# Kernel tuning notes

Hardware: AMD Instinct MI355X
Metric: run time of the kernel (lower is better)

## Reference

```python
import jax, jax.numpy as jnp
import numpy as np

DIM = 1024
NUM_HEADS = 16
HEAD_DIM = DIM // NUM_HEADS


def setup_inputs() -> dict:
    key = jax.random.key(0)
    k_x, k_qkv, k_proj, k_b = jax.random.split(key, 4)
    B, N, P, C = 4, 96, 64, DIM
    x = jax.random.normal(k_x, (B, N, P, C), dtype=jnp.float32)
    # nn.Linear(dim, 3*dim, bias=False): store as (in, out) for x @ W
    s = 1.0 / np.sqrt(C)
    W_qkv = jax.random.uniform(k_qkv, (C, 3 * C), minval=-s, maxval=s, dtype=jnp.float32)
    W_proj = jax.random.uniform(k_proj, (C, C), minval=-s, maxval=s, dtype=jnp.float32)
    b_proj = jax.random.uniform(k_b, (C,), minval=-s, maxval=s, dtype=jnp.float32)
    return {"x": x, "W_qkv": W_qkv, "W_proj": W_proj, "b_proj": b_proj}


def reference(x, W_qkv, W_proj, b_proj):
    B, N, P, C = x.shape
    H, hd = NUM_HEADS, C // NUM_HEADS
    # qkv projection: (B,N,P,3C) -> (B,N,P,3,H,hd)
    qkv = (x @ W_qkv).reshape(B, N, P, 3, H, hd)
    # q,k: mean-pool over patches P -> (B,H,N,hd)
    q = qkv[..., 0, :, :].mean(axis=2).transpose(0, 2, 1, 3)
    k = qkv[..., 1, :, :].mean(axis=2).transpose(0, 2, 1, 3)
    # v keeps all patches: (B,N,P,H,hd) -> (B,H,N,hd,P) -> (B,H,N,hd*P)
    v = qkv[..., 2, :, :].transpose(0, 3, 1, 4, 2).reshape(B, H, N, hd * P)
    # SDPA with default scale 1/sqrt(q_last_dim) = 1/sqrt(hd)
    scores = jnp.einsum('bhnd,bhmd->bhnm', q, k) * (hd ** -0.5)
    attn = jax.nn.softmax(scores, axis=-1)
    out = jnp.einsum('bhnm,bhme->bhne', attn, v)  # e = hd*P
    # unflatten back to (B,N,P,C)
    out = out.reshape(B, H, N, hd, P).transpose(0, 2, 4, 1, 3).reshape(B, N, P, C)
    return out @ W_proj + b_proj
```

## Files before the change

kernel.cpp:

```cpp
#include <hip/hip_runtime.h>
#include <cstdint>
#include <cstddef>

#define PPP  64
#define CC   1024

typedef __attribute__((ext_vector_type(8))) short short8;
typedef __attribute__((ext_vector_type(4))) float floatx4;
typedef __attribute__((ext_vector_type(4))) unsigned short ushort4v;

__device__ inline float bf2f(unsigned short u) {
  union { unsigned int i; float f; } v; v.i = ((unsigned int)u) << 16; return v.f;
}
__device__ inline unsigned short f2bf(float f) {
  union { float f; unsigned int i; } v; v.f = f;
  unsigned int x = v.i;
  unsigned int r = (x + 0x7fffu + ((x >> 16) & 1u)) >> 16;
  return (unsigned short)r;
}

#define GLD16(gp, lp)                                                          \
  __builtin_amdgcn_global_load_lds(                                            \
      (const __attribute__((address_space(1))) void*)(gp),                     \
      (__attribute__((address_space(3))) void*)(lp), 16, 0, 0)

__global__ __launch_bounds__(256) void conv_mean(
    const float* __restrict__ x, unsigned short* __restrict__ xbf,
    unsigned short* __restrict__ xm) {
  int bn = blockIdx.x;
  int c4 = threadIdx.x * 4;
  const float* xp = x + (size_t)bn * (PPP * CC) + c4;
  unsigned short* xo = xbf + (size_t)bn * (PPP * CC) + c4;
  float4 s = {0.f, 0.f, 0.f, 0.f};
#pragma unroll 8
  for (int p = 0; p < PPP; ++p) {
    float4 v = *(const float4*)&xp[(size_t)p * CC];
    s.x += v.x; s.y += v.y; s.z += v.z; s.w += v.w;
    ushort4v pk;
    pk.x = f2bf(v.x); pk.y = f2bf(v.y); pk.z = f2bf(v.z); pk.w = f2bf(v.w);
    *(ushort4v*)&xo[(size_t)p * CC] = pk;
  }
  ushort4v pm;
  pm.x = f2bf(s.x * (1.0f / PPP)); pm.y = f2bf(s.y * (1.0f / PPP));
  pm.z = f2bf(s.z * (1.0f / PPP)); pm.w = f2bf(s.w * (1.0f / PPP));
  *(ushort4v*)&xm[(size_t)bn * CC + c4] = pm;
}

__global__ __launch_bounds__(256) void transpose_f32_bf16(
    const float* __restrict__ src, unsigned short* __restrict__ dst,
    int R, int Cc, int src_stride) {
  __shared__ unsigned short tile[32][33];
  int tc = blockIdx.x * 32, tr = blockIdx.y * 32;
  int tx = threadIdx.x & 31, ty = threadIdx.x >> 5;
  for (int yy = ty; yy < 32; yy += 8)
    tile[yy][tx] = f2bf(src[(size_t)(tr + yy) * src_stride + tc + tx]);
  __syncthreads();
  for (int yy = ty; yy < 32; yy += 8)
    dst[(size_t)(tc + yy) * R + tr + tx] = tile[tx][yy];
}

template <bool F32OUT, bool SWIZ>
__global__ __launch_bounds__(256) void gemm_bt(
    const unsigned short* __restrict__ A, const unsigned short* __restrict__ BT,
    void* __restrict__ Cout, const float* __restrict__ bias,
    int M, int N, int K, int nbx) {
  __shared__ unsigned short As[128 * 32];
  __shared__ unsigned short Bs[128 * 32];

  int bx, by;
  {
    int bid = blockIdx.x;
    if (SWIZ) {
      bx = (bid >> 3) & 7;
      by = (bid & 7) * (gridDim.x >> 6) + (bid >> 6);
    } else {
      bx = bid % nbx;
      by = bid / nbx;
    }
  }
  const int rowBase = by * 128;
  const int colBase = bx * 128;
  const int t = threadIdx.x;
  const int wave = t >> 6, lane = t & 63;
  const int qr = wave >> 1, qc = wave & 1;
  const int m16 = lane & 15, quad = lane >> 4;

  floatx4 acc[4][4];
#pragma unroll
  for (int i = 0; i < 4; ++i)
#pragma unroll
    for (int j = 0; j < 4; ++j) {
      acc[i][j][0] = 0.f; acc[i][j][1] = 0.f; acc[i][j][2] = 0.f; acc[i][j][3] = 0.f;
    }

  for (int k0 = 0; k0 < K; k0 += 32) {
    __syncthreads();
#pragma unroll
    for (int u = 0; u < 2; ++u) {
      int ch = (u * 4 + wave) * 64 + lane;
      int row = ch >> 2, c8 = (ch & 3) << 3;
      GLD16(&A [(size_t)(rowBase + row) * K + k0 + c8], &As[ch * 8]);
      GLD16(&BT[(size_t)(colBase + row) * K + k0 + c8], &Bs[ch * 8]);
    }
    __syncthreads();

    short8 af[4], bfr[4];
#pragma unroll
    for (int i = 0; i < 4; ++i)
      af[i] = *(const short8*)&As[(qr * 64 + i * 16 + m16) * 32 + quad * 8];
#pragma unroll
    for (int j = 0; j < 4; ++j)
      bfr[j] = *(const short8*)&Bs[(qc * 64 + j * 16 + m16) * 32 + quad * 8];
#pragma unroll
    for (int i = 0; i < 4; ++i)
#pragma unroll
      for (int j = 0; j < 4; ++j)
        acc[i][j] = __builtin_amdgcn_mfma_f32_16x16x32_bf16(af[i], bfr[j], acc[i][j], 0, 0, 0);
  }

  float bv[4];
#pragma unroll
  for (int j = 0; j < 4; ++j)
    bv[j] = bias ? bias[colBase + qc * 64 + j * 16 + m16] : 0.f;

#pragma unroll
  for (int i = 0; i < 4; ++i) {
    int row0 = rowBase + qr * 64 + i * 16 + quad * 4;
#pragma unroll
    for (int j = 0; j < 4; ++j) {
      int col = colBase + qc * 64 + j * 16 + m16;
#pragma unroll
      for (int r = 0; r < 4; ++r) {
        float f = acc[i][j][r] + bv[j];
        if (F32OUT)
          ((float*)Cout)[(size_t)(row0 + r) * N + col] = f;
        else
          ((unsigned short*)Cout)[(size_t)(row0 + r) * N + col] = f2bf(f);
      }
    }
  }
}

__global__ __launch_bounds__(128) void softmax_k(
    const float* __restrict__ qk, unsigned short* __restrict__ attn) {
  int bh = blockIdx.x;
  int b = bh >> 4, h = bh & 15;
  __shared__ float ks[96][64];
  __shared__ float sc[96][96];
  int t = threadIdx.x;
  for (int idx = t; idx < 96 * 64; idx += 128) {
    int n = idx >> 6, d = idx & 63;
    ks[n][d] = qk[(size_t)(b * 96 + n) * 2048 + 1024 + h * 64 + d];
  }
  __syncthreads();
  if (t < 96) {
    float qreg[64];
    const float* qrow = qk + (size_t)(b * 96 + t) * 2048 + h * 64;
#pragma unroll
    for (int d = 0; d < 64; ++d) qreg[d] = qrow[d];

    float mx = -1e30f;
    for (int m = 0; m < 96; ++m) {
      float s0 = 0.f, s1 = 0.f, s2 = 0.f, s3 = 0.f;
#pragma unroll
      for (int d = 0; d < 64; d += 4) {
        s0 += qreg[d + 0] * ks[m][d + 0];
        s1 += qreg[d + 1] * ks[m][d + 1];
        s2 += qreg[d + 2] * ks[m][d + 2];
        s3 += qreg[d + 3] * ks[m][d + 3];
      }
      float s = ((s0 + s1) + (s2 + s3)) * 0.125f;
      sc[m][t] = s;
      mx = fmaxf(mx, s);
    }
    float sum = 0.f;
    for (int m = 0; m < 96; ++m) {
      float e = __expf(sc[m][t] - mx);
      sc[m][t] = e;
      sum += e;
    }
    float inv = 1.0f / sum;
    size_t base = (size_t)(bh * 96 + t) * 96;
    for (int m = 0; m < 96; ++m) attn[base + m] = f2bf(sc[m][t] * inv);
  }
}

__global__ __launch_bounds__(256) void attn_apply_mfma(
    const unsigned short* __restrict__ attn, const unsigned short* __restrict__ V,
    unsigned short* __restrict__ out2) {
  const int bid = blockIdx.x;
  const int bh = bid >> 5, ct = bid & 31;
  const int b = bh >> 4;
  const int t = threadIdx.x;
  const int wave = t >> 6, lane = t & 63;
  const int m16 = lane & 15, quad = lane >> 4;

  const unsigned short* An = attn + (size_t)bh * 96 * 96;
  const int vb = b * 96 * 64 * CC;

  floatx4 acc[6][2];
#pragma unroll
  for (int i = 0; i < 6; ++i)
#pragma unroll
    for (int j = 0; j < 2; ++j) {
      acc[i][j][0] = 0.f; acc[i][j][1] = 0.f; acc[i][j][2] = 0.f; acc[i][j][3] = 0.f;
    }

  int p_[2], base_[2];
#pragma unroll
  for (int jj = 0; jj < 2; ++jj) {
    int colL = wave * 32 + jj * 16;
    int p = ct * 2 + (colL >> 6);
    int d = (colL & 63) + m16;
    p_[jj] = p;
    base_[jj] = vb + p * CC + ((bh & 15) * 64) + d;
  }

#pragma unroll
  for (int k0 = 0; k0 < 96; k0 += 32) {
    short8 af[6];
#pragma unroll
    for (int i = 0; i < 6; ++i)
      af[i] = *(const short8*)&An[(i * 16 + m16) * 96 + k0 + quad * 8];
#pragma unroll
    for (int jj = 0; jj < 2; ++jj) {
      short8 bfr;
#pragma unroll
      for (int j = 0; j < 8; ++j)
        bfr[j] = (short)V[(size_t)base_[jj] + (size_t)(k0 + quad * 8 + j) * (64 * CC)];
#pragma unroll
      for (int i = 0; i < 6; ++i)
        acc[i][jj] = __builtin_amdgcn_mfma_f32_16x16x32_bf16(af[i], bfr, acc[i][jj], 0, 0, 0);
    }
  }

#pragma unroll
  for (int jj = 0; jj < 2; ++jj) {
    int colL = wave * 32 + jj * 16;
    int d = (colL & 63) + m16;
    size_t obase = (size_t)(b * 96) * 64 * CC + (size_t)p_[jj] * CC + (bh & 15) * 64 + d;
#pragma unroll
    for (int i = 0; i < 6; ++i) {
#pragma unroll
      for (int r = 0; r < 4; ++r) {
        int n = i * 16 + quad * 4 + r;
        out2[obase + (size_t)n * (64 * CC)] = f2bf(acc[i][jj][r]);
      }
    }
  }
}

extern "C" void kernel_launch(void* const* d_in, const int* in_sizes, int n_in,
                              void* d_out, int out_size, void* d_ws, size_t ws_size,
                              hipStream_t stream) {
  const float* x      = (const float*)d_in[0];
  const float* W_qkv  = (const float*)d_in[1];
  const float* W_proj = (const float*)d_in[2];
  const float* b_proj = (const float*)d_in[3];
  float* out = (float*)d_out;

  char* w = (char*)d_ws;
  unsigned short* WqkvT = (unsigned short*)(w);
  unsigned short* WpT   = (unsigned short*)(w + 6291456);
  unsigned short* xm    = (unsigned short*)(w + 8388608);
  float*          qkbuf = (float*)(w + 9175040);
  unsigned short* attn  = (unsigned short*)(w + 12320768);
  unsigned short* out2w = (unsigned short*)(w + 13500416);
  unsigned short* xbf   = (unsigned short*)d_out;
  unsigned short* Vbuf  = (unsigned short*)((char*)d_out + 50331648);

  const bool fullws = ws_size >= (size_t)13500416 + 50331648;

  conv_mean<<<dim3(384), 256, 0, stream>>>(x, xbf, xm);

  transpose_f32_bf16<<<dim3(96, 32), 256, 0, stream>>>(W_qkv, WqkvT, 1024, 3072, 3072);
  transpose_f32_bf16<<<dim3(32, 32), 256, 0, stream>>>(W_proj, WpT, 1024, 1024, 1024);

  gemm_bt<true, false><<<dim3(48), 256, 0, stream>>>(
      xm, WqkvT, qkbuf, nullptr, 384, 2048, 1024, 16);

  softmax_k<<<dim3(64), 128, 0, stream>>>(qkbuf, attn);

  gemm_bt<false, true><<<dim3(1536), 256, 0, stream>>>(
      xbf, WqkvT + (size_t)2048 * 1024, Vbuf, nullptr, 24576, 1024, 1024, 8);

  if (fullws) {
    attn_apply_mfma<<<dim3(2048), 256, 0, stream>>>(attn, Vbuf, out2w);
    gemm_bt<true, true><<<dim3(1536), 256, 0, stream>>>(
        out2w, WpT, out, b_proj, 24576, 1024, 1024, 8);
  } else {
    for (int b = 0; b < 4; ++b) {
      attn_apply_mfma<<<dim3(512), 256, 0, stream>>>(
          attn + (size_t)b * 16 * 96 * 96,
          Vbuf + (size_t)b * 6144 * 1024,
          out2w);
      gemm_bt<true, true><<<dim3(384), 256, 0, stream>>>(
          out2w, WpT, out + (size_t)b * 6144 * 1024, b_proj, 6144, 1024, 1024, 8);
    }
  }
}
```

Baseline: 407.5 us.

## Add 256x128-tile triple-buffered MFMA GEMM for the large V and output projections

```diff
diff --git a/kernel.cpp b/kernel.cpp
--- a/kernel.cpp
+++ b/kernel.cpp
@@ -141,6 +141,149 @@
   }
 }
 
+template <bool F32OUT>
+__global__ __launch_bounds__(512, 2) void gemm_bt256(
+    const unsigned short* __restrict__ A, const unsigned short* __restrict__ BT,
+    void* __restrict__ Cout, const float* __restrict__ bias,
+    int M, int N, int K) {
+  __shared__ __attribute__((aligned(16))) unsigned short As[3][256 * 64];
+  __shared__ __attribute__((aligned(16))) unsigned short Bs[3][128 * 64];
+
+  const int nbx = N >> 7;
+  int tid = (blockIdx.x & 7) * (gridDim.x >> 3) + (blockIdx.x >> 3);
+  const int bx = tid % nbx, by = tid / nbx;
+  const int rowBase = by * 256;
+  const int colBase = bx * 128;
+
+  const int t = threadIdx.x;
+  const int wave = t >> 6, lane = t & 63;
+  const int wr = wave >> 1, wc = wave & 1;
+  const int m16 = lane & 15, quad = lane >> 4;
+  const int sw7 = lane & 7;
+
+  const unsigned short* srcA[4];
+  const unsigned short* srcB[2];
+  int offA[4], offB[2];
+#pragma unroll
+  for (int u = 0; u < 4; ++u) {
+    int c = (u * 8 + wave) * 64 + lane;
+    int row = c >> 3, pch = c & 7;
+    int l = pch ^ (row & 7);
+    srcA[u] = A + (size_t)(rowBase + row) * K + l * 8;
+    offA[u] = c * 8;
+  }
+#pragma unroll
+  for (int u = 0; u < 2; ++u) {
+    int c = (u * 8 + wave) * 64 + lane;
+    int row = c >> 3, pch = c & 7;
+    int l = pch ^ (row & 7);
+    srcB[u] = BT + (size_t)(colBase + row) * K + l * 8;
+    offB[u] = c * 8;
+  }
+
+  floatx4 acc[4][4];
+#pragma unroll
+  for (int i = 0; i < 4; ++i)
+#pragma unroll
+    for (int j = 0; j < 4; ++j) {
+      acc[i][j][0] = 0.f; acc[i][j][1] = 0.f; acc[i][j][2] = 0.f; acc[i][j][3] = 0.f;
+    }
+
+  const int NT = K >> 6;
+
+#pragma unroll
+  for (int u = 0; u < 4; ++u) GLD16(srcA[u], &As[0][offA[u]]);
+#pragma unroll
+  for (int u = 0; u < 2; ++u) GLD16(srcB[u], &Bs[0][offB[u]]);
+#pragma unroll
+  for (int u = 0; u < 4; ++u) GLD16(srcA[u] + 64, &As[1][offA[u]]);
+#pragma unroll
+  for (int u = 0; u < 2; ++u) GLD16(srcB[u] + 64, &Bs[1][offB[u]]);
+
+#define LDA_F(Ac, i, kh) \
+  (*(const short8*)&(Ac)[(wr * 64 + (i) * 16 + m16) * 64 + ((((kh) * 4 + quad) ^ sw7) * 8)])
+#define LDB_F(Bc, j, kh) \
+  (*(const short8*)&(Bc)[(wc * 64 + (j) * 16 + m16) * 64 + ((((kh) * 4 + quad) ^ sw7) * 8)])
+
+  int cur = 0, nb = 2;
+#pragma unroll 1
+  for (int kt = 0; kt < NT; ++kt) {
+    if (kt == NT - 1)
+      asm volatile("s_waitcnt vmcnt(0)" ::: "memory");
+    else
+      asm volatile("s_waitcnt vmcnt(6)" ::: "memory");
+    asm volatile("s_barrier" ::: "memory");
+
+    const unsigned short* Ac = &As[cur][0];
+    const unsigned short* Bc = &Bs[cur][0];
+    const bool st = (kt + 2) < NT;
+    const int koff = (kt + 2) << 6;
+
+#pragma unroll
+    for (int p = 0; p < 4; ++p) {
+      const int i0 = (p >> 1) * 2, i1 = i0 + 1;
+      const int j0 = (p & 1) * 2, j1 = j0 + 1;
+      short8 A00 = LDA_F(Ac, i0, 0), A01 = LDA_F(Ac, i0, 1);
+      short8 A10 = LDA_F(Ac, i1, 0), A11 = LDA_F(Ac, i1, 1);
+      short8 B00 = LDB_F(Bc, j0, 0), B01 = LDB_F(Bc, j0, 1);
+      short8 B10 = LDB_F(Bc, j1, 0), B11 = LDB_F(Bc, j1, 1);
+      if (st) {
+        if (p == 0) {
+          GLD16(srcA[0] + koff, &As[nb][offA[0]]);
+          GLD16(srcA[1] + koff, &As[nb][offA[1]]);
+        } else if (p == 1) {
+          GLD16(srcA[2] + koff, &As[nb][offA[2]]);
+          GLD16(srcA[3] + koff, &As[nb][offA[3]]);
+        } else if (p == 2) {
+          GLD16(srcB[0] + koff, &Bs[nb][offB[0]]);
+        } else {
+          GLD16(srcB[1] + koff, &Bs[nb][offB[1]]);
+        }
+      }
+      asm volatile("s_barrier" ::: "memory");
+      __builtin_amdgcn_sched_barrier(0);
+      __builtin_amdgcn_s_setprio(1);
+      acc[i0][j0] = __builtin_amdgcn_mfma_f32_16x16x32_bf16(A00, B00, acc[i0][j0], 0, 0, 0);
+      acc[i0][j0] = __builtin_amdgcn_mfma_f32_16x16x32_bf16(A01, B01, acc[i0][j0], 0, 0, 0);
+      acc[i0][j1] = __builtin_amdgcn_mfma_f32_16x16x32_bf16(A00, B10, acc[i0][j1], 0, 0, 0);
+      acc[i0][j1] = __builtin_amdgcn_mfma_f32_16x16x32_bf16(A01, B11, acc[i0][j1], 0, 0, 0);
+      acc[i1][j0] = __builtin_amdgcn_mfma_f32_16x16x32_bf16(A10, B00, acc[i1][j0], 0, 0, 0);
+      acc[i1][j0] = __builtin_amdgcn_mfma_f32_16x16x32_bf16(A11, B01, acc[i1][j0], 0, 0, 0);
+      acc[i1][j1] = __builtin_amdgcn_mfma_f32_16x16x32_bf16(A10, B10, acc[i1][j1], 0, 0, 0);
+      acc[i1][j1] = __builtin_amdgcn_mfma_f32_16x16x32_bf16(A11, B11, acc[i1][j1], 0, 0, 0);
+      __builtin_amdgcn_s_setprio(0);
+      __builtin_amdgcn_sched_barrier(0);
+      asm volatile("s_barrier" ::: "memory");
+    }
+    cur = (cur == 2) ? 0 : cur + 1;
+    nb = (nb == 2) ? 0 : nb + 1;
+  }
+#undef LDA_F
+#undef LDB_F
+
+  float bv[4];
+#pragma unroll
+  for (int j = 0; j < 4; ++j)
+    bv[j] = bias ? bias[colBase + wc * 64 + j * 16 + m16] : 0.f;
+
+#pragma unroll
+  for (int i = 0; i < 4; ++i) {
+    int row0 = rowBase + wr * 64 + i * 16 + quad * 4;
+#pragma unroll
+    for (int j = 0; j < 4; ++j) {
+      int col = colBase + wc * 64 + j * 16 + m16;
+#pragma unroll
+      for (int r = 0; r < 4; ++r) {
+        float f = acc[i][j][r] + bv[j];
+        if (F32OUT)
+          ((float*)Cout)[(size_t)(row0 + r) * N + col] = f;
+        else
+          ((unsigned short*)Cout)[(size_t)(row0 + r) * N + col] = f2bf(f);
+      }
+    }
+  }
+}
+
 __global__ __launch_bounds__(128) void softmax_k(
     const float* __restrict__ qk, unsigned short* __restrict__ attn) {
   int bh = blockIdx.x;
@@ -281,21 +424,21 @@
 
   softmax_k<<<dim3(64), 128, 0, stream>>>(qkbuf, attn);
 
-  gemm_bt<false, true><<<dim3(1536), 256, 0, stream>>>(
-      xbf, WqkvT + (size_t)2048 * 1024, Vbuf, nullptr, 24576, 1024, 1024, 8);
+  gemm_bt256<false><<<dim3(768), 512, 0, stream>>>(
+      xbf, WqkvT + (size_t)2048 * 1024, Vbuf, nullptr, 24576, 1024, 1024);
 
   if (fullws) {
     attn_apply_mfma<<<dim3(2048), 256, 0, stream>>>(attn, Vbuf, out2w);
-    gemm_bt<true, true><<<dim3(1536), 256, 0, stream>>>(
-        out2w, WpT, out, b_proj, 24576, 1024, 1024, 8);
+    gemm_bt256<true><<<dim3(768), 512, 0, stream>>>(
+        out2w, WpT, out, b_proj, 24576, 1024, 1024);
   } else {
     for (int b = 0; b < 4; ++b) {
       attn_apply_mfma<<<dim3(512), 256, 0, stream>>>(
           attn + (size_t)b * 16 * 96 * 96,
           Vbuf + (size_t)b * 6144 * 1024,
           out2w);
-      gemm_bt<true, true><<<dim3(384), 256, 0, stream>>>(
-          out2w, WpT, out + (size_t)b * 6144 * 1024, b_proj, 6144, 1024, 1024, 8);
-    }
-  }
-}
+      gemm_bt256<true><<<dim3(192), 512, 0, stream>>>(
+          out2w, WpT, out + (size_t)b * 6144 * 1024, b_proj, 6144, 1024, 1024);
+    }
+  }
+}
```

Result: slower. 434.5 us (+6.6%).

## Add 256x256-tile bf16 GEMM with phased double-buffered pipeline for V and proj

Applied to the files above, without the earlier changes.

```diff
diff --git a/kernel.cpp b/kernel.cpp
--- a/kernel.cpp
+++ b/kernel.cpp
@@ -141,6 +141,161 @@
   }
 }
 
+template <bool F32OUT>
+__global__ __launch_bounds__(512, 2) void gemm_bt256(
+    const unsigned short* __restrict__ A, const unsigned short* __restrict__ BT,
+    void* __restrict__ Cout, const float* __restrict__ bias,
+    int M, int N, int K) {
+  __shared__ __attribute__((aligned(16))) unsigned short As[2][256 * 64];
+  __shared__ __attribute__((aligned(16))) unsigned short Bs[2][256 * 64];
+
+  const int nbx = N >> 8;
+  int tid = (blockIdx.x & 7) * (gridDim.x >> 3) + (blockIdx.x >> 3);
+  const int bx = tid % nbx, by = tid / nbx;
+  const int rowBase = by * 256, colBase = bx * 256;
+
+  const int t = threadIdx.x;
+  const int wave = t >> 6, lane = t & 63;
+  const int wr = wave >> 2, wc = wave & 3;
+  const int m16 = lane & 15, quad = lane >> 4;
+  const int sw7 = m16 & 7;
+
+  const unsigned short* srcA[4];
+  int offA[4];
+#pragma unroll
+  for (int u = 0; u < 4; ++u) {
+    int c = u * 512 + t;
+    int row = c >> 3, pch = c & 7;
+    int l = pch ^ (row & 7);
+    srcA[u] = A + (size_t)(rowBase + row) * K + l * 8;
+    offA[u] = c * 8;
+  }
+  const unsigned short* srcB[2][2];
+  int offB[2][2];
+#pragma unroll
+  for (int g = 0; g < 2; ++g)
+#pragma unroll
+    for (int u = 0; u < 2; ++u) {
+      int i = u * 512 + t;
+      int col = g * 32 + ((i >> 8) << 6) + ((i >> 3) & 31);
+      int kcp = i & 7;
+      int l = kcp ^ (col & 7);
+      srcB[g][u] = BT + (size_t)(colBase + col) * K + l * 8;
+      offB[g][u] = col * 64 + kcp * 8;
+    }
+
+  floatx4 acc[8][4];
+#pragma unroll
+  for (int i = 0; i < 8; ++i)
+#pragma unroll
+    for (int j = 0; j < 4; ++j) {
+      acc[i][j][0] = 0.f; acc[i][j][1] = 0.f; acc[i][j][2] = 0.f; acc[i][j][3] = 0.f;
+    }
+
+  short8 ar[4][2];
+  short8 br[2][2][2];
+
+#define RD_A(buf, qa)                                                          \
+  _Pragma("unroll") for (int i_ = 0; i_ < 4; ++i_)                             \
+  _Pragma("unroll") for (int kh_ = 0; kh_ < 2; ++kh_)                          \
+    ar[i_][kh_] = *(const short8*)&As[buf][                                    \
+        (wr * 128 + (qa) * 64 + i_ * 16 + m16) * 64 +                          \
+        (((kh_ * 4 + quad) ^ sw7) * 8)];
+#define RD_B(buf, qb)                                                          \
+  _Pragma("unroll") for (int j_ = 0; j_ < 2; ++j_)                             \
+  _Pragma("unroll") for (int kh_ = 0; kh_ < 2; ++kh_)                          \
+    br[qb][j_][kh_] = *(const short8*)&Bs[buf][                                \
+        (wc * 64 + (qb) * 32 + j_ * 16 + m16) * 64 +                           \
+        (((kh_ * 4 + quad) ^ sw7) * 8)];
+#define MFMA_PH(qa, qb)                                                        \
+  __builtin_amdgcn_sched_barrier(0);                                           \
+  __builtin_amdgcn_s_setprio(1);                                               \
+  _Pragma("unroll") for (int kh_ = 0; kh_ < 2; ++kh_)                          \
+  _Pragma("unroll") for (int i_ = 0; i_ < 4; ++i_)                             \
+  _Pragma("unroll") for (int j_ = 0; j_ < 2; ++j_)                             \
+    acc[(qa) * 4 + i_][(qb) * 2 + j_] =                                        \
+        __builtin_amdgcn_mfma_f32_16x16x32_bf16(                               \
+            ar[i_][kh_], br[qb][j_][kh_], acc[(qa) * 4 + i_][(qb) * 2 + j_],   \
+            0, 0, 0);                                                          \
+  __builtin_amdgcn_s_setprio(0);                                               \
+  __builtin_amdgcn_sched_barrier(0);
+#define WAITV(n) asm volatile("s_waitcnt vmcnt(" #n ")" ::: "memory")
+#define BAR() asm volatile("s_barrier" ::: "memory")
+
+  GLD16(srcA[0], &As[0][offA[0]]);
+  GLD16(srcA[2], &As[0][offA[2]]);
+  GLD16(srcB[0][0], &Bs[0][offB[0][0]]);
+  GLD16(srcB[0][1], &Bs[0][offB[0][1]]);
+  GLD16(srcB[1][0], &Bs[0][offB[1][0]]);
+  GLD16(srcB[1][1], &Bs[0][offB[1][1]]);
+  GLD16(srcA[1], &As[0][offA[1]]);
+  GLD16(srcA[3], &As[0][offA[3]]);
+
+  const int NT = K >> 6;
+  int cur = 0;
+#pragma unroll 1
+  for (int kt = 0; kt < NT - 1; ++kt, cur ^= 1) {
+    const int nxt = cur ^ 1;
+    const int ko = (kt + 1) << 6;
+    WAITV(4); BAR();
+    RD_A(cur, 0); RD_B(cur, 0);
+    GLD16(srcA[0] + ko, &As[nxt][offA[0]]);
+    GLD16(srcA[2] + ko, &As[nxt][offA[2]]);
+    MFMA_PH(0, 0);
+    WAITV(4); BAR();
+    RD_B(cur, 1);
+    GLD16(srcB[0][0] + ko, &Bs[nxt][offB[0][0]]);
+    GLD16(srcB[0][1] + ko, &Bs[nxt][offB[0][1]]);
+    MFMA_PH(0, 1);
+    WAITV(4); BAR();
+    RD_A(cur, 1);
+    GLD16(srcB[1][0] + ko, &Bs[nxt][offB[1][0]]);
+    GLD16(srcB[1][1] + ko, &Bs[nxt][offB[1][1]]);
+    MFMA_PH(1, 0);
+    GLD16(srcA[1] + ko, &As[nxt][offA[1]]);
+    GLD16(srcA[3] + ko, &As[nxt][offA[3]]);
+    MFMA_PH(1, 1);
+  }
+  WAITV(4); BAR();
+  RD_A(cur, 0); RD_B(cur, 0);
+  MFMA_PH(0, 0);
+  WAITV(2); BAR();
+  RD_B(cur, 1);
+  MFMA_PH(0, 1);
+  WAITV(0); BAR();
+  RD_A(cur, 1);
+  MFMA_PH(1, 0);
+  MFMA_PH(1, 1);
+
+#undef RD_A
+#undef RD_B
+#undef MFMA_PH
+#undef WAITV
+#undef BAR
+
+  float bv[4];
+#pragma unroll
+  for (int jg = 0; jg < 4; ++jg)
+    bv[jg] = bias ? bias[colBase + wc * 64 + jg * 16 + m16] : 0.f;
+
+#pragma unroll
+  for (int ig = 0; ig < 8; ++ig) {
+    int row0 = rowBase + wr * 128 + ig * 16 + quad * 4;
+#pragma unroll
+    for (int jg = 0; jg < 4; ++jg) {
+      int col = colBase + wc * 64 + jg * 16 + m16;
+#pragma unroll
+      for (int r = 0; r < 4; ++r) {
+        float f = acc[ig][jg][r] + bv[jg];
+        if (F32OUT)
+          ((float*)Cout)[(size_t)(row0 + r) * N + col] = f;
+        else
+          ((unsigned short*)Cout)[(size_t)(row0 + r) * N + col] = f2bf(f);
+      }
+    }
+  }
+}
+
 __global__ __launch_bounds__(128) void softmax_k(
     const float* __restrict__ qk, unsigned short* __restrict__ attn) {
   int bh = blockIdx.x;
@@ -281,21 +436,21 @@
 
   softmax_k<<<dim3(64), 128, 0, stream>>>(qkbuf, attn);
 
-  gemm_bt<false, true><<<dim3(1536), 256, 0, stream>>>(
-      xbf, WqkvT + (size_t)2048 * 1024, Vbuf, nullptr, 24576, 1024, 1024, 8);
+  gemm_bt256<false><<<dim3(384), 512, 0, stream>>>(
+      xbf, WqkvT + (size_t)2048 * 1024, Vbuf, nullptr, 24576, 1024, 1024);
 
   if (fullws) {
     attn_apply_mfma<<<dim3(2048), 256, 0, stream>>>(attn, Vbuf, out2w);
-    gemm_bt<true, true><<<dim3(1536), 256, 0, stream>>>(
-        out2w, WpT, out, b_proj, 24576, 1024, 1024, 8);
+    gemm_bt256<true><<<dim3(384), 512, 0, stream>>>(
+        out2w, WpT, out, b_proj, 24576, 1024, 1024);
   } else {
     for (int b = 0; b < 4; ++b) {
       attn_apply_mfma<<<dim3(512), 256, 0, stream>>>(
           attn + (size_t)b * 16 * 96 * 96,
           Vbuf + (size_t)b * 6144 * 1024,
           out2w);
-      gemm_bt<true, true><<<dim3(384), 256, 0, stream>>>(
-          out2w, WpT, out + (size_t)b * 6144 * 1024, b_proj, 6144, 1024, 1024, 8);
-    }
-  }
-}
+      gemm_bt256<true><<<dim3(96), 512, 0, stream>>>(
+          out2w, WpT, out + (size_t)b * 6144 * 1024, b_proj, 6144, 1024, 1024);
+    }
+  }
+}
```

Result: faster. 386.5 us (-5.2%).

## Add 128x256-tile double-buffered bf16 GEMM for the two large projections

Applied to the files above, without the earlier changes.

```diff
diff --git a/kernel.cpp b/kernel.cpp
--- a/kernel.cpp
+++ b/kernel.cpp
@@ -141,6 +141,113 @@
   }
 }
 
+template <bool F32OUT>
+__global__ __launch_bounds__(256, 2) void gemm_bt128(
+    const unsigned short* __restrict__ A, const unsigned short* __restrict__ BT,
+    void* __restrict__ Cout, const float* __restrict__ bias,
+    int M, int N, int K) {
+  __shared__ __attribute__((aligned(16))) unsigned short As[2][128 * 32];
+  __shared__ __attribute__((aligned(16))) unsigned short Bs[2][256 * 32];
+
+  const int nbx = N >> 8;
+  int tid = (blockIdx.x & 7) * (gridDim.x >> 3) + (blockIdx.x >> 3);
+  const int bx = tid % nbx, by = tid / nbx;
+  const int rowBase = by * 128, colBase = bx * 256;
+
+  const int t = threadIdx.x;
+  const int wave = t >> 6, lane = t & 63;
+  const int m16 = lane & 15, quad = lane >> 4;
+  const int ck = quad ^ ((m16 >> 1) & 3);
+
+  const unsigned short* srcA[2]; int offA[2];
+#pragma unroll
+  for (int u = 0; u < 2; ++u) {
+    int c = u * 256 + t;
+    int row = c >> 2, pch = c & 3;
+    int l = pch ^ ((row >> 1) & 3);
+    srcA[u] = A + (size_t)(rowBase + row) * K + l * 8;
+    offA[u] = c * 8;
+  }
+  const unsigned short* srcB[4]; int offB[4];
+#pragma unroll
+  for (int u = 0; u < 4; ++u) {
+    int c = u * 256 + t;
+    int row = c >> 2, pch = c & 3;
+    int l = pch ^ ((row >> 1) & 3);
+    srcB[u] = BT + (size_t)(colBase + row) * K + l * 8;
+    offB[u] = c * 8;
+  }
+
+  floatx4 acc[8][4];
+#pragma unroll
+  for (int i = 0; i < 8; ++i)
+#pragma unroll
+    for (int j = 0; j < 4; ++j) {
+      acc[i][j][0] = 0.f; acc[i][j][1] = 0.f; acc[i][j][2] = 0.f; acc[i][j][3] = 0.f;
+    }
+
+#define WAITV0() asm volatile("s_waitcnt vmcnt(0)" ::: "memory")
+#define BARR()   asm volatile("s_barrier" ::: "memory")
+
+#pragma unroll
+  for (int u = 0; u < 2; ++u) GLD16(srcA[u], &As[0][offA[u]]);
+#pragma unroll
+  for (int u = 0; u < 4; ++u) GLD16(srcB[u], &Bs[0][offB[u]]);
+
+  const int NT = K >> 5;
+  int cur = 0;
+#pragma unroll 1
+  for (int kt = 0; kt < NT; ++kt, cur ^= 1) {
+    WAITV0(); BARR();
+    if (kt + 1 < NT) {
+      const int ko = (kt + 1) << 5;
+      const int nxt = cur ^ 1;
+#pragma unroll
+      for (int u = 0; u < 2; ++u) GLD16(srcA[u] + ko, &As[nxt][offA[u]]);
+#pragma unroll
+      for (int u = 0; u < 4; ++u) GLD16(srcB[u] + ko, &Bs[nxt][offB[u]]);
+    }
+    short8 af[8], bfr[4];
+#pragma unroll
+    for (int i = 0; i < 8; ++i)
+      af[i] = *(const short8*)&As[cur][(i * 16 + m16) * 32 + ck * 8];
+#pragma unroll
+    for (int j = 0; j < 4; ++j)
+      bfr[j] = *(const short8*)&Bs[cur][(wave * 64 + j * 16 + m16) * 32 + ck * 8];
+    __builtin_amdgcn_s_setprio(1);
+#pragma unroll
+    for (int i = 0; i < 8; ++i)
+#pragma unroll
+      for (int j = 0; j < 4; ++j)
+        acc[i][j] = __builtin_amdgcn_mfma_f32_16x16x32_bf16(af[i], bfr[j], acc[i][j], 0, 0, 0);
+    __builtin_amdgcn_s_setprio(0);
+  }
+#undef WAITV0
+#undef BARR
+
+  float bv[4];
+#pragma unroll
+  for (int jg = 0; jg < 4; ++jg)
+    bv[jg] = bias ? bias[colBase + wave * 64 + jg * 16 + m16] : 0.f;
+
+#pragma unroll
+  for (int ig = 0; ig < 8; ++ig) {
+    int row0 = rowBase + ig * 16 + quad * 4;
+#pragma unroll
+    for (int jg = 0; jg < 4; ++jg) {
+      int col = colBase + wave * 64 + jg * 16 + m16;
+#pragma unroll
+      for (int r = 0; r < 4; ++r) {
+        float f = acc[ig][jg][r] + bv[jg];
+        if (F32OUT)
+          ((float*)Cout)[(size_t)(row0 + r) * N + col] = f;
+        else
+          ((unsigned short*)Cout)[(size_t)(row0 + r) * N + col] = f2bf(f);
+      }
+    }
+  }
+}
+
 __global__ __launch_bounds__(128) void softmax_k(
     const float* __restrict__ qk, unsigned short* __restrict__ attn) {
   int bh = blockIdx.x;
@@ -281,21 +388,21 @@
 
   softmax_k<<<dim3(64), 128, 0, stream>>>(qkbuf, attn);
 
-  gemm_bt<false, true><<<dim3(1536), 256, 0, stream>>>(
-      xbf, WqkvT + (size_t)2048 * 1024, Vbuf, nullptr, 24576, 1024, 1024, 8);
+  gemm_bt128<false><<<dim3(768), 256, 0, stream>>>(
+      xbf, WqkvT + (size_t)2048 * 1024, Vbuf, nullptr, 24576, 1024, 1024);
 
   if (fullws) {
     attn_apply_mfma<<<dim3(2048), 256, 0, stream>>>(attn, Vbuf, out2w);
-    gemm_bt<true, true><<<dim3(1536), 256, 0, stream>>>(
-        out2w, WpT, out, b_proj, 24576, 1024, 1024, 8);
+    gemm_bt128<true><<<dim3(768), 256, 0, stream>>>(
+        out2w, WpT, out, b_proj, 24576, 1024, 1024);
   } else {
     for (int b = 0; b < 4; ++b) {
       attn_apply_mfma<<<dim3(512), 256, 0, stream>>>(
           attn + (size_t)b * 16 * 96 * 96,
           Vbuf + (size_t)b * 6144 * 1024,
           out2w);
-      gemm_bt<true, true><<<dim3(384), 256, 0, stream>>>(
-          out2w, WpT, out + (size_t)b * 6144 * 1024, b_proj, 6144, 1024, 1024, 8);
-    }
-  }
-}
+      gemm_bt128<true><<<dim3(192), 256, 0, stream>>>(
+          out2w, WpT, out + (size_t)b * 6144 * 1024, b_proj, 6144, 1024, 1024);
+    }
+  }
+}
```

New measurement: 418.3 us. 1.03x slower.
